# Optimization experiments

Measured on AMD Instinct MI355X. Metric: run time of the kernel, lower is better.

## Reference

```python
import jax, jax.numpy as jnp
import numpy as np

DIM = 2048
N_HEADS = 16
N_KV = 4
HEAD_DIM = DIM // N_HEADS  # 128
B, S = 2, 2048
EPS = float(np.finfo(np.float32).eps)  # torch RMSNorm eps=None -> finfo eps


def _rotate_half(x):
    # interleaved-pair rotation: out[..., ::2] = -x[..., 1::2]; out[..., 1::2] = x[..., ::2]
    x2 = x.reshape(x.shape[:-1] + (HEAD_DIM // 2, 2))
    rot = jnp.stack([-x2[..., 1], x2[..., 0]], axis=-1)
    return rot.reshape(x.shape)


def _rmsnorm(x, w):
    var = jnp.mean(x * x, axis=-1, keepdims=True)
    return x * jax.lax.rsqrt(var + EPS) * w


def setup_inputs() -> dict:
    key = jax.random.key(0)
    ks = jax.random.split(key, 5)
    out_f = (N_HEADS + 2 * N_KV) * HEAD_DIM  # 3072
    return {
        "x": jax.random.normal(ks[0], (B, S, DIM), jnp.float32),
        "wqkv": jax.random.normal(ks[1], (out_f, DIM), jnp.float32) * (2.0 / (DIM + out_f)) ** 0.5,
        "wo": jax.random.normal(ks[2], (DIM, DIM), jnp.float32) * (1.0 / DIM) ** 0.5,
        "q_norm_w": jnp.ones((HEAD_DIM,), jnp.float32),
        "k_norm_w": jnp.ones((HEAD_DIM,), jnp.float32),
        "freqs_cos": jnp.cos(jax.random.normal(ks[3], (S, 1, HEAD_DIM), jnp.float32)),
        "freqs_sin": jnp.sin(jax.random.normal(ks[4], (S, 1, HEAD_DIM), jnp.float32)),
    }


def reference(x, wqkv, wo, q_norm_w, k_norm_w, freqs_cos, freqs_sin):
    b, s, _ = x.shape
    qkv = jnp.einsum("bsd,od->bso", x, wqkv)
    q_size = N_HEADS * HEAD_DIM
    kv_size = N_KV * HEAD_DIM
    xq = qkv[..., :q_size].reshape(b, s, N_HEADS, HEAD_DIM)
    xk = qkv[..., q_size:q_size + kv_size].reshape(b, s, N_KV, HEAD_DIM)
    xv = qkv[..., q_size + kv_size:].reshape(b, s, N_KV, HEAD_DIM)
    xq = _rmsnorm(xq, q_norm_w)
    xk = _rmsnorm(xk, k_norm_w)
    # RoPE (freqs broadcast over batch and heads)
    xq = xq * freqs_cos + _rotate_half(xq) * freqs_sin
    xk = xk * freqs_cos + _rotate_half(xk) * freqs_sin
    # GQA: group query heads per kv head instead of materializing repeats
    rep = N_HEADS // N_KV
    q = xq.transpose(0, 2, 1, 3).reshape(b, N_KV, rep, s, HEAD_DIM)
    k = xk.transpose(0, 2, 1, 3)  # [b, kv, s, d]
    v = xv.transpose(0, 2, 1, 3)
    scale = 1.0 / jnp.sqrt(jnp.asarray(HEAD_DIM, x.dtype))
    scores = jnp.einsum("bhgqd,bhkd->bhgqk", q, k) * scale
    probs = jax.nn.softmax(scores, axis=-1)
    attn = jnp.einsum("bhgqk,bhkd->bhgqd", probs, v)
    attn = attn.reshape(b, N_HEADS, s, HEAD_DIM).transpose(0, 2, 1, 3).reshape(b, s, DIM)
    return jnp.einsum("bsd,od->bso", attn, wo)
```

## Files before the change

### kernel.cpp

```cpp
#include <hip/hip_runtime.h>
#include <hip/hip_bf16.h>

typedef unsigned short u16;
typedef __bf16 bf16x8 __attribute__((ext_vector_type(8)));
typedef __bf16 bf16x4 __attribute__((ext_vector_type(4)));
typedef u16 u16x8 __attribute__((ext_vector_type(8)));
typedef float f32x4 __attribute__((ext_vector_type(4)));
typedef float f32x16 __attribute__((ext_vector_type(16)));

__device__ __forceinline__ u16 f2bf(float f) {
    unsigned u = __float_as_uint(f);
    return (u16)((u + 0x7fffu + ((u >> 16) & 1u)) >> 16);
}
__device__ __forceinline__ unsigned pkbf2(float a, float b) {
    __hip_bfloat162 h = __float22bfloat162_rn(make_float2(a, b));
    return *(unsigned*)&h;
}

__device__ __forceinline__ void gload16(const u16* g, u16* l) {
    __builtin_amdgcn_global_load_lds(
        (const __attribute__((address_space(1))) void*)g,
        (__attribute__((address_space(3))) void*)l, 16, 0, 0);
}

__device__ __forceinline__ void block_sync() {
    __builtin_amdgcn_sched_barrier(0);
    __builtin_amdgcn_s_barrier();
    __builtin_amdgcn_sched_barrier(0);
}
template<int N> __device__ __forceinline__ void waitvm() {
    if constexpr (N == 0)      asm volatile("s_waitcnt vmcnt(0)" ::: "memory");
    else if constexpr (N == 6) asm volatile("s_waitcnt vmcnt(6)" ::: "memory");
    else                       asm volatile("s_waitcnt vmcnt(8)" ::: "memory");
}

__global__ void cvt_bf16(const float* __restrict__ src, u16* __restrict__ dst, int n4) {
    int i = blockIdx.x * 256 + threadIdx.x;
    if (i >= n4) return;
    float4 v = *(const float4*)(src + (size_t)i * 4);
    uint2 o; o.x = pkbf2(v.x, v.y); o.y = pkbf2(v.z, v.w);
    *(uint2*)(dst + (size_t)i * 4) = o;
}

template<int ROWS>
__device__ __forceinline__ void stage_tile(const u16* __restrict__ g, int K,
                                           int k0, u16* l, int tid) {
#pragma unroll
    for (int s = 0; s < ROWS / 64; ++s) {
        int row = s * 64 + (tid >> 3);
        int sc = (tid & 7) ^ ((tid >> 3) & 7);
        gload16(g + (size_t)row * K + k0 + sc * 8, l + s * 4096 + tid * 8);
    }
}

template<int BM, int BN>
__device__ __forceinline__ void gemm_pipeline(const u16* __restrict__ Ab,
                                              const u16* __restrict__ Bb, int K,
                                              u16* sAll,
                                              f32x4 (&acc)[BM / 32][BN / 64],
                                              int tid) {
    constexpr int MR = BM / 32, NR = BN / 64;
    constexpr int TILE = (BM + BN) * 64;
    const int lane = tid & 63, wave = tid >> 6;
    const int quad = lane >> 4, l16 = lane & 15;
    const int wm = wave >> 2, wn = wave & 3;
    const int ar0 = wm * (BM / 2) + l16;
    const int br0 = wn * (BN / 4) + l16;

    u16* sA0 = sAll;        u16* sB0 = sAll + BM * 64;
    u16* sA1 = sAll + TILE; u16* sB1 = sAll + TILE + BM * 64;

    stage_tile<BM>(Ab, K, 0, sA0, tid);
    stage_tile<BN>(Bb, K, 0, sB0, tid);

    const int nt = K >> 6;
    for (int t = 0; t < nt; ++t) {
        const u16* cA = (t & 1) ? sA1 : sA0;
        const u16* cB = (t & 1) ? sB1 : sB0;
        if (t + 1 < nt) {
            u16* nA = (t & 1) ? sA0 : sA1;
            u16* nB = (t & 1) ? sB0 : sB1;
            stage_tile<BM>(Ab, K, (t + 1) * 64, nA, tid);
            stage_tile<BN>(Bb, K, (t + 1) * 64, nB, tid);
            waitvm<(BM + BN) / 64>();
        } else {
            waitvm<0>();
        }
        block_sync();
#pragma unroll
        for (int kk = 0; kk < 2; ++kk) {
            const int c = kk * 4 + quad;
            bf16x8 af[MR], bf[NR];
#pragma unroll
            for (int m = 0; m < MR; ++m) {
                int r = ar0 + m * 16;
                af[m] = *(const bf16x8*)&cA[r * 64 + ((c ^ (r & 7)) * 8)];
            }
#pragma unroll
            for (int n = 0; n < NR; ++n) {
                int r = br0 + n * 16;
                bf[n] = *(const bf16x8*)&cB[r * 64 + ((c ^ (r & 7)) * 8)];
            }
            __builtin_amdgcn_s_setprio(1);
#pragma unroll
            for (int m = 0; m < MR; ++m)
#pragma unroll
                for (int n = 0; n < NR; ++n)
                    acc[m][n] = __builtin_amdgcn_mfma_f32_16x16x32_bf16(
                        af[m], bf[n], acc[m][n], 0, 0, 0);
            __builtin_amdgcn_s_setprio(0);
        }
        block_sync();
    }
}

__global__ __launch_bounds__(512, 2)
void gemm_bt(const u16* __restrict__ A, const u16* __restrict__ B,
             float* __restrict__ C, int M, int N, int K) {
    __shared__ u16 sAll[2 * (128 + 256) * 64];
    const int tid = threadIdx.x;
    const int wave = tid >> 6, lane = tid & 63;
    const int quad = lane >> 4, l16 = lane & 15;
    const int wm = wave >> 2, wn = wave & 3;
    const int bid = blockIdx.x;
    const int xcd = bid & 7, r2 = bid >> 3;
    const int bni = (xcd & 1) * 4 + (r2 & 3);
    const int bmi = (xcd >> 1) * 8 + (r2 >> 2);
    const size_t bm = (size_t)bmi * 128, bn = (size_t)bni * 256;
    f32x4 acc[4][4] = {};
    gemm_pipeline<128, 256>(A + bm * K, B + bn * K, K, sAll, acc, tid);
#pragma unroll
    for (int m = 0; m < 4; ++m)
#pragma unroll
        for (int n = 0; n < 4; ++n)
#pragma unroll
            for (int r = 0; r < 4; ++r)
                C[(bm + wm * 64 + m * 16 + quad * 4 + r) * (size_t)N +
                  bn + wn * 64 + n * 16 + l16] = acc[m][n][r];
}

__global__ __launch_bounds__(512, 2)
void gemm_qkv(const u16* __restrict__ xb, const u16* __restrict__ wq,
              const float* __restrict__ qw, const float* __restrict__ kw,
              const float* __restrict__ fcos, const float* __restrict__ fsin,
              u16* __restrict__ qb, u16* __restrict__ kb, u16* __restrict__ vt) {
    __shared__ u16 sAll[2 * (256 + 256) * 64];
    const int tid = threadIdx.x;
    const int wave = tid >> 6, lane = tid & 63;
    const int quad = lane >> 4, l16 = lane & 15;
    const int wm = wave >> 2, wn = wave & 3;
    const int bid = blockIdx.x;
    const int xcd = bid & 7, r2 = bid >> 3;
    const int bx = (xcd & 1) * 6 + r2 % 6;
    const int by = (xcd >> 1) * 4 + r2 / 6;
    f32x4 acc[8][4] = {};
    gemm_pipeline<256, 256>(xb + (size_t)by * 256 * 2048,
                            wq + (size_t)bx * 256 * 2048, 2048, sAll, acc, tid);

    const int b = by >> 3;
    const int sb = (by & 7) * 256 + wm * 128;
    const int headh = wn >> 1;
    const int dcol0 = (wn & 1) * 64;

    if (bx >= 10) {
        const int qp = ((quad & 1) << 1) | (quad >> 1);
        const int kvh = (bx - 10) * 2 + headh;
        u16* base = vt + (size_t)(b * 4 + kvh) * 128 * 2048;
#pragma unroll
        for (int m = 0; m < 8; ++m) {
            int s0 = sb + m * 16 + qp * 4;
#pragma unroll
            for (int n = 0; n < 4; ++n) {
                int d = dcol0 + n * 16 + l16;
                bf16x4 pv;
#pragma unroll
                for (int r = 0; r < 4; ++r) pv[r] = (__bf16)acc[m][n][r];
                *(bf16x4*)(base + (size_t)d * 2048 + s0) = pv;
            }
        }
        return;
    }

    float* red = (float*)sAll;
    float ssq[8][4];
#pragma unroll
    for (int m = 0; m < 8; ++m)
#pragma unroll
        for (int r = 0; r < 4; ++r) {
            float t = 0.f;
#pragma unroll
            for (int n = 0; n < 4; ++n) t += acc[m][n][r] * acc[m][n][r];
#pragma unroll
            for (int off = 1; off <= 8; off <<= 1) t += __shfl_xor(t, off);
            ssq[m][r] = t;
        }
    if (l16 == 0)
#pragma unroll
        for (int m = 0; m < 8; ++m)
#pragma unroll
            for (int r = 0; r < 4; ++r)
                red[((wn & 1) * 2 + headh) * 256 + wm * 128 + m * 16 + quad * 4 + r] =
                    ssq[m][r];
    __syncthreads();

    const bool isQ = bx < 8;
    const float qscl = isQ ? 0.08838834764831845f * 1.4426950408889634f : 1.0f;
    const float* wp = isQ ? qw : kw;
    float wcol[4];
#pragma unroll
    for (int n = 0; n < 4; ++n) wcol[n] = wp[dcol0 + n * 16 + l16];
    u16* dstbase = isQ ? qb + (size_t)(b * 16 + bx * 2 + headh) * 2048 * 128
                       : kb + (size_t)(b * 4 + (bx - 8) * 2 + headh) * 2048 * 128;
    const float sgn = (l16 & 1) ? 1.f : -1.f;

#pragma unroll
    for (int m = 0; m < 8; ++m) {
#pragma unroll
        for (int r = 0; r < 4; ++r) {
            int rowl = wm * 128 + m * 16 + quad * 4 + r;
            float var = (red[(0 + headh) * 256 + rowl] +
                         red[(2 + headh) * 256 + rowl]) * (1.0f / 128.0f);
            float rms = rsqrtf(var + 1.1920928955078125e-07f) * qscl;
            int s = sb + m * 16 + quad * 4 + r;
            const float* fc = fcos + (size_t)s * 128 + dcol0;
            const float* fn = fsin + (size_t)s * 128 + dcol0;
            u16* drow = dstbase + (size_t)s * 128 + dcol0;
#pragma unroll
            for (int n = 0; n < 4; ++n) {
                float y = acc[m][n][r] * rms * wcol[n];
                float yp = __shfl_xor(y, 1);
                float o = y * fc[n * 16 + l16] + sgn * yp * fn[n * 16 + l16];
                drow[n * 16 + l16] = f2bf(o);
            }
        }
    }
}

#define KBUF(c) ((c) * 8192)
#define VBUF(c) (16384 + (c) * 8192)
__global__ __launch_bounds__(256, 2)
void flash_attn(const u16* __restrict__ qb, const u16* __restrict__ kb,
                const u16* __restrict__ vt, u16* __restrict__ ab) {
    __shared__ u16 smem[32768];
    __shared__ float Llds[128];

    const int tid = threadIdx.x;
    const int wave = tid >> 6, lane = tid & 63;
    const int hf = lane >> 5, c32 = lane & 31;
    const int bid = blockIdx.x;
    const int swz = (bid & 7) * 64 + (bid >> 3);
    const int qt = swz & 15, bh = swz >> 4;
    const int hh = bh & 15, bb = bh >> 4;
    const int kh = hh >> 2;

    const u16* Qbase = qb + (size_t)(bb * 16 + hh) * 2048 * 128;
    const u16* Kbase = kb + (size_t)(bb * 4 + kh) * 2048 * 128;
    const u16* Vbase = vt + (size_t)(bb * 4 + kh) * 128 * 2048;

    bf16x8 aq[8];
#pragma unroll
    for (int kq = 0; kq < 8; ++kq)
        aq[kq] = *(const bf16x8*)(Qbase +
            (size_t)(qt * 128 + wave * 32 + c32) * 128 + kq * 16 + hf * 8);

    f32x16 O[4] = {};
    float lacc = 0.f;

    const int krow = tid >> 4;
    const u16* kg = Kbase + (size_t)krow * 128 + (((tid & 15) ^ (krow & 7)) * 8);
    const int vrow = tid >> 3;
    const u16* vg = Vbase + (size_t)vrow * 2048 + (((tid & 7) ^ (vrow & 7)) * 8);

    auto stage = [&](int buf, int key0) {
#pragma unroll
        for (int s = 0; s < 4; ++s) {
            gload16(kg + key0 * 128 + s * 2048, &smem[KBUF(buf) + s * 2048 + tid * 8]);
            gload16(vg + (size_t)s * 65536 + key0, &smem[VBUF(buf) + s * 2048 + tid * 8]);
        }
    };

    stage(0, 0);

    for (int kt = 0; kt < 32; ++kt) {
        const int cur = kt & 1, nxt = cur ^ 1;
        if (kt < 31) {
            stage(nxt, (kt + 1) * 64);
            waitvm<8>();
        } else {
            waitvm<0>();
        }
        block_sync();

        f32x16 sc[2] = {};
        __builtin_amdgcn_s_setprio(1);
#pragma unroll
        for (int kq = 0; kq < 8; ++kq) {
#pragma unroll
            for (int mt = 0; mt < 2; ++mt) {
                bf16x8 kf = *(const bf16x8*)&smem[KBUF(cur) + (mt * 32 + c32) * 128 +
                                                 (((kq * 2 + hf) ^ (c32 & 7)) * 8)];
                sc[mt] = __builtin_amdgcn_mfma_f32_32x32x16_bf16(kf, aq[kq], sc[mt], 0, 0, 0);
            }
        }
        __builtin_amdgcn_s_setprio(0);

        int pdw[2][8];
#pragma unroll
        for (int mt = 0; mt < 2; ++mt) {
            float p[16];
#pragma unroll
            for (int r = 0; r < 16; ++r) {
                p[r] = __builtin_amdgcn_exp2f(sc[mt][r]);
                lacc += p[r];
            }
#pragma unroll
            for (int i = 0; i < 8; ++i) pdw[mt][i] = (int)pkbf2(p[2 * i], p[2 * i + 1]);
        }

        __builtin_amdgcn_s_setprio(1);
#pragma unroll
        for (int kc = 0; kc < 4; ++kc) {
            const int mt = kc >> 1, L = kc & 1;
            union { int i[4]; bf16x8 v; } u;
            u.i[0] = pdw[mt][4 * L + 0];
            u.i[1] = pdw[mt][4 * L + 1];
            u.i[2] = pdw[mt][4 * L + 2];
            u.i[3] = pdw[mt][4 * L + 3];
#pragma unroll
            for (int dt = 0; dt < 4; ++dt) {
                bf16x8 vf = *(const bf16x8*)&smem[VBUF(cur) + (dt * 32 + c32) * 64 +
                                                 (((kc * 2 + hf) ^ (c32 & 7)) * 8)];
                O[dt] = __builtin_amdgcn_mfma_f32_32x32x16_bf16(u.v, vf, O[dt], 0, 0, 0);
            }
        }
        __builtin_amdgcn_s_setprio(0);
        block_sync();
    }

    float l = lacc + __shfl_xor(lacc, 32);
    if (hf == 0) Llds[wave * 32 + c32] = l;

    float inv[16];
#pragma unroll
    for (int r = 0; r < 16; ++r)
        inv[r] = __builtin_amdgcn_rcpf(Llds[wave * 32 + (r & 3) + 8 * (r >> 2) + 4 * hf]);

    u16* scr = &smem[wave * 32 * 136];
#pragma unroll
    for (int dt = 0; dt < 4; ++dt)
#pragma unroll
        for (int r = 0; r < 16; ++r) {
            int q_r = (r & 3) + 8 * (r >> 2) + 4 * hf;
            scr[q_r * 136 + dt * 32 + c32] = f2bf(O[dt][r] * inv[r]);
        }
#pragma unroll
    for (int it = 0; it < 8; ++it) {
        int f = it * 64 + lane;
        int row = f >> 4, c = f & 15;
        u16x8 v = *(const u16x8*)&scr[row * 136 + c * 8];
        int qg = qt * 128 + wave * 32 + row;
        *(u16x8*)(ab + ((size_t)(bb * 2048 + qg)) * 2048 + hh * 128 + c * 8) = v;
    }
}

extern "C" void kernel_launch(void* const* d_in, const int* in_sizes, int n_in,
                              void* d_out, int out_size, void* d_ws, size_t ws_size,
                              hipStream_t stream) {
    const float* x    = (const float*)d_in[0];
    const float* wqkv = (const float*)d_in[1];
    const float* wo   = (const float*)d_in[2];
    const float* qw   = (const float*)d_in[3];
    const float* kw   = (const float*)d_in[4];
    const float* fc   = (const float*)d_in[5];
    const float* fs   = (const float*)d_in[6];
    float* out = (float*)d_out;
    char* ws = (char*)d_ws;

    u16* xb    = (u16*)(ws + 0);
    u16* wqkvb = (u16*)(ws + 16777216);
    u16* wob   = (u16*)(ws + 29360128);
    u16* qb    = (u16*)(ws + 37748736);
    u16* kb    = (u16*)(ws + 54525952);
    u16* vt    = (u16*)(ws + 58720256);
    u16* ab    = (u16*)(ws + 62914560);

    cvt_bf16<<<8192, 256, 0, stream>>>(x, xb, 2097152);
    cvt_bf16<<<6144, 256, 0, stream>>>(wqkv, wqkvb, 1572864);
    cvt_bf16<<<4096, 256, 0, stream>>>(wo, wob, 1048576);
    gemm_qkv<<<192, 512, 0, stream>>>(xb, wqkvb, qw, kw, fc, fs, qb, kb, vt);
    flash_attn<<<512, 256, 0, stream>>>(qb, kb, vt, ab);
    gemm_bt<<<256, 512, 0, stream>>>(ab, wob, out, 4096, 2048, 2048);
}
```

Baseline: 305.2 us.

## Single-buffer V in flash attention for 3 blocks/CU and fuse bf16 conversions

V now uses a single LDS buffer and K keeps its double buffer, cutting shared memory from 64KB to 48KB so launch bounds can rise to 3 blocks per CU. The next V tile is loaded after the PV MFMAs, with an extra vmcnt wait and barrier before the PV stage. The three fp32-to-bf16 conversion launches become one grid-stride kernel, and the row-sum accumulation becomes a tree reduction. V latency is now less hidden and there is an extra barrier per iteration, traded for higher occupancy and fewer kernel launches.

```diff
diff --git a/kernel.cpp b/kernel.cpp
--- a/kernel.cpp
+++ b/kernel.cpp
@@ -30,16 +30,26 @@
 }
 template<int N> __device__ __forceinline__ void waitvm() {
     if constexpr (N == 0)      asm volatile("s_waitcnt vmcnt(0)" ::: "memory");
+    else if constexpr (N == 4) asm volatile("s_waitcnt vmcnt(4)" ::: "memory");
     else if constexpr (N == 6) asm volatile("s_waitcnt vmcnt(6)" ::: "memory");
     else                       asm volatile("s_waitcnt vmcnt(8)" ::: "memory");
 }
 
-__global__ void cvt_bf16(const float* __restrict__ src, u16* __restrict__ dst, int n4) {
-    int i = blockIdx.x * 256 + threadIdx.x;
-    if (i >= n4) return;
-    float4 v = *(const float4*)(src + (size_t)i * 4);
-    uint2 o; o.x = pkbf2(v.x, v.y); o.y = pkbf2(v.z, v.w);
-    *(uint2*)(dst + (size_t)i * 4) = o;
+#define CVT_N1 2097152
+#define CVT_N2 3670016
+#define CVT_TOT 4718592
+__global__ void cvt_all(const float* __restrict__ x, const float* __restrict__ wqkv,
+                        const float* __restrict__ wo, u16* __restrict__ xb,
+                        u16* __restrict__ wqkvb, u16* __restrict__ wob) {
+    for (int i = blockIdx.x * 256 + threadIdx.x; i < CVT_TOT; i += 4608 * 256) {
+        const float* s; u16* d; int j;
+        if (i < CVT_N1)      { s = x;    d = xb;    j = i; }
+        else if (i < CVT_N2) { s = wqkv; d = wqkvb; j = i - CVT_N1; }
+        else                 { s = wo;   d = wob;   j = i - CVT_N2; }
+        float4 v = *(const float4*)(s + (size_t)j * 4);
+        uint2 o; o.x = pkbf2(v.x, v.y); o.y = pkbf2(v.z, v.w);
+        *(uint2*)(d + (size_t)j * 4) = o;
+    }
 }
 
 template<int ROWS>
@@ -237,11 +247,11 @@
 }
 
 #define KBUF(c) ((c) * 8192)
-#define VBUF(c) (16384 + (c) * 8192)
-__global__ __launch_bounds__(256, 2)
+#define VBUF 16384
+__global__ __launch_bounds__(256, 3)
 void flash_attn(const u16* __restrict__ qb, const u16* __restrict__ kb,
                 const u16* __restrict__ vt, u16* __restrict__ ab) {
-    __shared__ u16 smem[32768];
+    __shared__ u16 smem[24576];
     __shared__ float Llds[128];
 
     const int tid = threadIdx.x;
@@ -271,20 +281,24 @@
     const int vrow = tid >> 3;
     const u16* vg = Vbase + (size_t)vrow * 2048 + (((tid & 7) ^ (vrow & 7)) * 8);
 
-    auto stage = [&](int buf, int key0) {
-#pragma unroll
-        for (int s = 0; s < 4; ++s) {
+    auto stageK = [&](int buf, int key0) {
+#pragma unroll
+        for (int s = 0; s < 4; ++s)
             gload16(kg + key0 * 128 + s * 2048, &smem[KBUF(buf) + s * 2048 + tid * 8]);
-            gload16(vg + (size_t)s * 65536 + key0, &smem[VBUF(buf) + s * 2048 + tid * 8]);
-        }
     };
-
-    stage(0, 0);
+    auto stageV = [&](int key0) {
+#pragma unroll
+        for (int s = 0; s < 4; ++s)
+            gload16(vg + (size_t)s * 65536 + key0, &smem[VBUF + s * 2048 + tid * 8]);
+    };
+
+    stageK(0, 0);
+    stageV(0);
 
     for (int kt = 0; kt < 32; ++kt) {
-        const int cur = kt & 1, nxt = cur ^ 1;
+        const int cur = kt & 1;
         if (kt < 31) {
-            stage(nxt, (kt + 1) * 64);
+            stageK(cur ^ 1, (kt + 1) * 64);
             waitvm<8>();
         } else {
             waitvm<0>();
@@ -309,13 +323,19 @@
         for (int mt = 0; mt < 2; ++mt) {
             float p[16];
 #pragma unroll
-            for (int r = 0; r < 16; ++r) {
-                p[r] = __builtin_amdgcn_exp2f(sc[mt][r]);
-                lacc += p[r];
-            }
+            for (int r = 0; r < 16; ++r) p[r] = __builtin_amdgcn_exp2f(sc[mt][r]);
+            float a0 = (p[0] + p[1]) + (p[2] + p[3]);
+            float a1 = (p[4] + p[5]) + (p[6] + p[7]);
+            float a2 = (p[8] + p[9]) + (p[10] + p[11]);
+            float a3 = (p[12] + p[13]) + (p[14] + p[15]);
+            lacc += (a0 + a1) + (a2 + a3);
 #pragma unroll
             for (int i = 0; i < 8; ++i) pdw[mt][i] = (int)pkbf2(p[2 * i], p[2 * i + 1]);
         }
+
+        if (kt < 31) waitvm<4>();
+        else         waitvm<0>();
+        block_sync();
 
         __builtin_amdgcn_s_setprio(1);
 #pragma unroll
@@ -328,13 +348,14 @@
             u.i[3] = pdw[mt][4 * L + 3];
 #pragma unroll
             for (int dt = 0; dt < 4; ++dt) {
-                bf16x8 vf = *(const bf16x8*)&smem[VBUF(cur) + (dt * 32 + c32) * 64 +
+                bf16x8 vf = *(const bf16x8*)&smem[VBUF + (dt * 32 + c32) * 64 +
                                                  (((kc * 2 + hf) ^ (c32 & 7)) * 8)];
                 O[dt] = __builtin_amdgcn_mfma_f32_32x32x16_bf16(u.v, vf, O[dt], 0, 0, 0);
             }
         }
         __builtin_amdgcn_s_setprio(0);
         block_sync();
+        if (kt < 31) stageV((kt + 1) * 64);
     }
 
     float l = lacc + __shfl_xor(lacc, 32);
@@ -384,9 +405,7 @@
     u16* vt    = (u16*)(ws + 58720256);
     u16* ab    = (u16*)(ws + 62914560);
 
-    cvt_bf16<<<8192, 256, 0, stream>>>(x, xb, 2097152);
-    cvt_bf16<<<6144, 256, 0, stream>>>(wqkv, wqkvb, 1572864);
-    cvt_bf16<<<4096, 256, 0, stream>>>(wo, wob, 1048576);
+    cvt_all<<<4608, 256, 0, stream>>>(x, wqkv, wo, xb, wqkvb, wob);
     gemm_qkv<<<192, 512, 0, stream>>>(xb, wqkvb, qw, kw, fc, fs, qb, kb, vt);
     flash_attn<<<512, 256, 0, stream>>>(qb, kb, vt, ab);
     gemm_bt<<<256, 512, 0, stream>>>(ab, wob, out, 4096, 2048, 2048);
```

Measured after the change: 300.1 us. Within noise of the previous version (-1.7%).
